# Kernel tuning notes

Hardware: AMD Instinct MI355X
Metric: run time of the kernel (lower is better)

The kernel has to match this reference:

```python
import jax, jax.numpy as jnp
import numpy as np

B, S, HID, H, DK = 16, 1024, 512, 8, 64
NEG = -1e30


def setup_inputs() -> dict:
    key = jax.random.key(0)
    kx, kl, kq, kk, kv, ko = jax.random.split(key, 6)
    x = jax.random.normal(kx, (B, S, HID), dtype=jnp.float32)
    # mask is a prefix of ones per sample (the torch code fills nmask[i, :nsum, :nsum])
    lengths = jax.random.randint(kl, (B,), S // 2, S + 1)
    mask = (jnp.arange(S)[None, :] < lengths[:, None]).astype(jnp.int32)
    scale = 0.02
    Wq = jax.random.normal(kq, (H, HID, DK), dtype=jnp.float32) * scale  # stacked per-head Linear weights
    Wk = jax.random.normal(kk, (H, HID, DK), dtype=jnp.float32) * scale
    Wv = jax.random.normal(kv, (H, HID, DK), dtype=jnp.float32) * scale
    Wout = jax.random.normal(ko, (H * DK, HID), dtype=jnp.float32) * scale
    return {"x": x, "mask": mask, "Wq": Wq, "Wk": Wk, "Wv": Wv, "Wout": Wout}


def reference(x, mask, Wq, Wk, Wv, Wout):
    # x: [B,S,HID], mask: [B,S] int prefix mask
    nsum = mask.sum(-1).astype(jnp.float32)          # [B]
    valid = mask.astype(bool)                         # [B,S]
    pair = valid[:, :, None] & valid[:, None, :]      # [B,S,S] == nmask from the torch loop
    # batched per-head projections (equivalent to the per-head Linear loop)
    Q = jnp.einsum('bsh,nhd->bnsd', x, Wq)            # [B,H,S,DK]
    K = jnp.einsum('bsh,nhd->bnsd', x, Wk)
    V = jnp.einsum('bsh,nhd->bnsd', x, Wv)
    scores = jnp.einsum('bnqd,bnkd->bnqk', Q, K)      # [B,H,S,S]
    scores = scores / jnp.sqrt(nsum)[:, None, None, None]  # per-sample sqrt(len) scale
    scores = jnp.where(pair[:, None, :, :], scores, NEG)   # masked_softmax: -1e30 at masked slots
    p = jax.nn.softmax(scores, axis=-1)
    attn = jnp.einsum('bnqk,bnkd->bnqd', p, V)        # [B,H,S,DK]
    h = attn.transpose(0, 2, 1, 3).reshape(B, S, H * DK)  # concat heads along feature dim
    return jnp.einsum('bsf,fh->bsh', h, Wout)         # W_out, no bias
```

## Files before the change

kernel.cpp:

```cpp
#include <hip/hip_runtime.h>
#include <math.h>

constexpr int CB = 16;
constexpr int CS = 1024;
constexpr int CHID = 512;
constexpr int CH = 8;
constexpr int CDK = 64;

typedef _Float16 f16;
typedef __attribute__((ext_vector_type(8))) _Float16 f16x8;
typedef __attribute__((ext_vector_type(4))) _Float16 f16x4;
typedef __attribute__((ext_vector_type(4))) float f32x4;
typedef __attribute__((ext_vector_type(4))) unsigned int u32x4;
typedef __attribute__((ext_vector_type(2))) unsigned int u32x2;

__device__ inline f32x4 mfma16(f16x8 a, f16x8 b, f32x4 c) {
  return __builtin_amdgcn_mfma_f32_16x16x32_f16(a, b, c, 0, 0, 0);
}

__device__ inline void gld16(const void* g, void* l) {
  __builtin_amdgcn_global_load_lds(
      (const __attribute__((address_space(1))) void*)g,
      (__attribute__((address_space(3))) void*)l, 16, 0, 0);
}

__device__ inline float fast_exp2(float x) {
#if __has_builtin(__builtin_amdgcn_exp2f)
  return __builtin_amdgcn_exp2f(x);
#else
  return __expf(x * 0.6931471805599453f);
#endif
}

__device__ inline unsigned pack_rne(float a, float b) {
  union { f16 h[2]; unsigned u; } c;
  c.h[0] = (f16)a;
  c.h[1] = (f16)b;
  return c.u;
}

__device__ inline void quad_transpose(unsigned& x, unsigned& y) {
#if __has_builtin(__builtin_amdgcn_permlane32_swap) && \
    __has_builtin(__builtin_amdgcn_permlane16_swap)
  u32x2 a = __builtin_amdgcn_permlane32_swap(x, y, false, false);
  u32x2 b = __builtin_amdgcn_permlane16_swap(a[0], a[1], false, false);
  x = b[0];
  y = b[1];
#else
  asm volatile(
      "s_nop 1\n\t"
      "v_permlane32_swap_b32 %0, %1\n\t"
      "s_nop 1\n\t"
      "v_permlane16_swap_b32 %0, %1\n\t"
      "s_nop 1"
      : "+v"(x), "+v"(y));
#endif
}

#define LOG2E 1.4426950408889634f

__global__ __launch_bounds__(256) void prep_kernel(const float4* __restrict__ x,
                                                   f16x4* __restrict__ xh,
                                                   const int* __restrict__ mask,
                                                   int* __restrict__ lens,
                                                   float* __restrict__ Vsum) {
  const int bid = blockIdx.x, t = threadIdx.x;
  __shared__ int red[256];
  if (bid < 8192) {
    const int idx = bid * 256 + t;
    const float4 v = x[idx];
    f16x4 o;
    o[0] = (f16)v.x; o[1] = (f16)v.y; o[2] = (f16)v.z; o[3] = (f16)v.w;
    xh[idx] = o;
  } else {
    const int b = bid - 8192;
    const int g = b * 256 + t;
    Vsum[g * 2] = 0.f;
    Vsum[g * 2 + 1] = 0.f;
    int s = 0;
    for (int i = t; i < CS; i += 256) s += mask[b * CS + i];
    red[t] = s;
    __syncthreads();
    for (int off = 128; off > 0; off >>= 1) {
      if (t < off) red[t] += red[t + off];
      __syncthreads();
    }
    if (t == 0) lens[b] = red[0];
  }
}

__global__ __launch_bounds__(256) void cast_w_kernel(const float* __restrict__ Wq,
                                                     const float* __restrict__ Wk,
                                                     const float* __restrict__ Wv,
                                                     const float* __restrict__ Wout,
                                                     f16* __restrict__ wtAll) {
  const int y = blockIdx.y, kb = blockIdx.x, t = threadIdx.x;
  const int k0 = kb * 64;
  const float* src;
  int ldsrc;
  f16* dst;
  if (y < 24) {
    const int which = y >> 3, h = y & 7;
    const float* W = (which == 0) ? Wq : (which == 1) ? Wk : Wv;
    src = W + (size_t)h * 32768 + (size_t)k0 * 64;
    ldsrc = 64;
    dst = wtAll + (size_t)which * 262144 + (size_t)h * 32768;
  } else {
    const int c = y - 24;
    src = Wout + (size_t)k0 * 512 + c * 64;
    ldsrc = 512;
    dst = wtAll + (size_t)3 * 262144 + (size_t)c * 64 * 512;
  }

  __shared__ float Ts[64][68];
  {
    const int kr = t >> 4, cg = (t & 15) * 4;
#pragma unroll
    for (int rr = 0; rr < 4; ++rr) {
      const float4 v = *(const float4*)&src[(size_t)(rr * 16 + kr) * ldsrc + cg];
      Ts[rr * 16 + kr][cg] = v.x;
      Ts[rr * 16 + kr][cg + 1] = v.y;
      Ts[rr * 16 + kr][cg + 2] = v.z;
      Ts[rr * 16 + kr][cg + 3] = v.w;
    }
  }
  __syncthreads();
  {
    const int n = t >> 2, seg = t & 3;
    f16x8 a, b;
#pragma unroll
    for (int j = 0; j < 8; ++j) {
      a[j] = (f16)Ts[seg * 16 + j][n];
      b[j] = (f16)Ts[seg * 16 + 8 + j][n];
    }
    f16* d = &dst[(size_t)n * 512 + k0 + seg * 16];
    *(f16x8*)d = a;
    *(f16x8*)(d + 8) = b;
  }
}

__global__ __launch_bounds__(256) void qkvf_kernel(
    const f16* __restrict__ xh, const f16* __restrict__ wtAll,
    const int* __restrict__ lens, f16* __restrict__ Qh, f16* __restrict__ Kh,
    f16* __restrict__ Vth, float* __restrict__ Vsum) {
  const int ct = blockIdx.x, rt = blockIdx.y;
  const int which = ct >> 2, hp = ct & 3;
  const f16* Wt = wtAll + (size_t)which * 262144 + (size_t)hp * 65536;
  const int row0 = rt * 128;
  const int b = row0 >> 10, s0 = row0 & 1023;
  const int h0 = hp * 2;
  const int t = threadIdx.x;
  const int w = t >> 6, lane = t & 63, quad = lane >> 4, lcol = lane & 15;
  const int wr = w >> 1, wc = w & 1;

  __shared__ union SM {
    struct { f16 Xs[128][64]; f16 Ws[128][64]; } a;
    f16 Ts[128][136];
  } sm;

  f32x4 acc[4][4];
#pragma unroll
  for (int i = 0; i < 4; ++i)
#pragma unroll
    for (int j = 0; j < 4; ++j) acc[i][j] = (f32x4){0.f, 0.f, 0.f, 0.f};

  for (int k0 = 0; k0 < CHID; k0 += 64) {
    __syncthreads();
#pragma unroll
    for (int i = 0; i < 4; ++i) {
      const int c = t + 256 * i, r = c >> 3, sg = c & 7;
      const int gsw = (sg ^ (r & 7)) * 8;
      gld16(&xh[(size_t)(row0 + r) * CHID + k0 + gsw],
            (char*)&sm.a.Xs[0][0] + c * 16);
      gld16(&Wt[(size_t)r * CHID + k0 + gsw], (char*)&sm.a.Ws[0][0] + c * 16);
    }
    __syncthreads();

    f16x8 bf0[4], bf1[4];
#pragma unroll
    for (int j = 0; j < 4; ++j) {
      const int br = wc * 64 + j * 16 + lcol;
      bf0[j] = *(const f16x8*)&sm.a.Ws[br][(quad ^ (br & 7)) * 8];
      bf1[j] = *(const f16x8*)&sm.a.Ws[br][((quad ^ 4) ^ (br & 7)) * 8];
    }
#pragma unroll
    for (int i = 0; i < 4; ++i) {
      const int ar = wr * 64 + i * 16 + lcol;
      const f16x8 af0 = *(const f16x8*)&sm.a.Xs[ar][(quad ^ (ar & 7)) * 8];
      const f16x8 af1 =
          *(const f16x8*)&sm.a.Xs[ar][((quad ^ 4) ^ (ar & 7)) * 8];
#pragma unroll
      for (int j = 0; j < 4; ++j) {
        acc[i][j] = mfma16(af0, bf0[j], acc[i][j]);
        acc[i][j] = mfma16(af1, bf1[j], acc[i][j]);
      }
    }
  }

  if (which == 2) {
#pragma unroll
    for (int j = 0; j < 4; ++j) {
      float ps = 0.f;
#pragma unroll
      for (int i = 0; i < 4; ++i)
#pragma unroll
        for (int rr = 0; rr < 4; ++rr) ps += acc[i][j][rr];
      ps += __shfl_xor(ps, 16);
      ps += __shfl_xor(ps, 32);
      if (quad == 0) {
        const int d128 = wc * 64 + j * 16 + lcol;
        const int h = h0 + (d128 >> 6), d = d128 & 63;
        atomicAdd(&Vsum[((size_t)b * CH + h) * CDK + d], ps);
      }
    }
    __syncthreads();
#pragma unroll
    for (int i = 0; i < 4; ++i)
#pragma unroll
      for (int j = 0; j < 4; ++j) {
        f16x4 v4;
#pragma unroll
        for (int rr = 0; rr < 4; ++rr) v4[rr] = (f16)acc[i][j][rr];
        *(f16x4*)&sm.Ts[wc * 64 + j * 16 + lcol][wr * 64 + i * 16 + quad * 4] =
            v4;
      }
    __syncthreads();
    const int c16 = t & 15;
#pragma unroll
    for (int p = 0; p < 8; ++p) {
      const int vr = p * 16 + (t >> 4);
      const int h = h0 + (vr >> 6), d = vr & 63;
      *(f16x8*)&Vth[(((size_t)b * CH + h) * CDK + d) * CS + s0 + c16 * 8] =
          *(const f16x8*)&sm.Ts[vr][c16 * 8];
    }
  } else {
    const float qsc = (which == 0) ? rsqrtf((float)lens[b]) * LOG2E : 1.0f;
    __syncthreads();
#pragma unroll
    for (int i = 0; i < 4; ++i)
#pragma unroll
      for (int j = 0; j < 4; ++j)
#pragma unroll
        for (int rr = 0; rr < 4; ++rr)
          sm.Ts[wr * 64 + i * 16 + quad * 4 + rr][wc * 64 + j * 16 + lcol] =
              (f16)(acc[i][j][rr] * qsc);
    __syncthreads();
    f16* O = (which == 0) ? Qh : Kh;
    const int c8 = t & 7;
#pragma unroll
    for (int p = 0; p < 4; ++p) {
      const int row = p * 32 + (t >> 3);
#pragma unroll
      for (int half = 0; half < 2; ++half) {
        const int h = h0 + half;
        *(f16x8*)&O[(((size_t)b * CH + h) * CS + s0 + row) * CDK + c8 * 8] =
            *(const f16x8*)&sm.Ts[row][half * 64 + c8 * 8];
      }
    }
  }
}

__global__ __launch_bounds__(512, 4) void attn_kernel(
    const f16* __restrict__ Qh, const f16* __restrict__ Kh,
    const f16* __restrict__ Vth, const int* __restrict__ lens,
    const float* __restrict__ Vsum, f16* __restrict__ Hbh) {
  const int id = blockIdx.x;
  const int h = id & 7;
  const int slot = id >> 3;
  const int qt = slot & 3;
  const int b = slot >> 2;
  const int n = lens[b];
  const int t = threadIdx.x, w = t >> 6, lane = t & 63, quad = lane >> 4,
            lcol = lane & 15;

  const size_t bh = ((size_t)b * CH + h) * CS;
  const size_t bhd = ((size_t)b * CH + h) * CDK;

  const int nt = (n + 63) >> 6;
  const int rem = n & 63;
  const int ntm = rem ? nt - 1 : nt;

  __shared__ union SM {
    struct { f16 Ks[2][64][72]; f16 Vs[2][64][72]; } kv;
    f16 St[8][32][72];
  } sm;

  const int qbase = qt * 256 + w * 32;
  f16x8 qa[2][2];
#pragma unroll
  for (int set = 0; set < 2; ++set) {
    const size_t qr = bh + qbase + set * 16 + lcol;
    qa[set][0] = *(const f16x8*)&Qh[qr * CDK + quad * 8];
    qa[set][1] = *(const f16x8*)&Qh[qr * CDK + 32 + quad * 8];
  }

  f16x8 vones;
#pragma unroll
  for (int j = 0; j < 8; ++j) vones[j] = (f16)1.0f;

  f32x4 o[2][4];
#pragma unroll
  for (int set = 0; set < 2; ++set)
#pragma unroll
    for (int dt = 0; dt < 4; ++dt) o[set][dt] = (f32x4){0.f, 0.f, 0.f, 0.f};
  f32x4 o_l[2] = {(f32x4){0.f, 0.f, 0.f, 0.f}, (f32x4){0.f, 0.f, 0.f, 0.f}};

  const int sr = t >> 3, sg = t & 7;

  f16x8 pk, pv;
  pk = *(const f16x8*)&Kh[(bh + sr) * CDK + sg * 8];
  pv = *(const f16x8*)&Vth[(bhd + sr) * CS + sg * 8];
  *(f16x8*)&sm.kv.Ks[0][sr][sg * 8] = pk;
  *(f16x8*)&sm.kv.Vs[0][sr][sg * 8] = pv;
  __syncthreads();

  auto ktile = [&](const int kt, const bool masked) __attribute__((always_inline)) {
    const int cur = kt & 1, nxt = cur ^ 1;
    const int ktn = (kt + 1 < nt) ? kt + 1 : kt;
    pk = *(const f16x8*)&Kh[(bh + ktn * 64 + sr) * CDK + sg * 8];
    pv = *(const f16x8*)&Vth[(bhd + sr) * CS + ktn * 64 + sg * 8];

    f16x8 pa[2][2];
#pragma unroll
    for (int set = 0; set < 2; ++set) {
      f32x4 st[4];
#pragma unroll
      for (int ct = 0; ct < 4; ++ct) {
        const f16x8 kb0 = *(const f16x8*)&sm.kv.Ks[cur][ct * 16 + lcol][quad * 8];
        const f16x8 kb1 =
            *(const f16x8*)&sm.kv.Ks[cur][ct * 16 + lcol][32 + quad * 8];
        st[ct] = mfma16(kb0, qa[set][0], (f32x4){0.f, 0.f, 0.f, 0.f});
        st[ct] = mfma16(kb1, qa[set][1], st[ct]);
      }
      unsigned pkd[4][2];
#pragma unroll
      for (int c = 0; c < 4; ++c) {
        float p[4];
#pragma unroll
        for (int r = 0; r < 4; ++r) {
          float e = fast_exp2(st[c][r]);
          if (masked) {
            const bool kvld = (kt * 64 + c * 16 + quad * 4 + r) < n;
            e = kvld ? e : 0.f;
          }
          p[r] = e;
        }
        pkd[c][0] = pack_rne(p[0], p[1]);
        pkd[c][1] = pack_rne(p[2], p[3]);
      }
#pragma unroll
      for (int half = 0; half < 2; ++half) {
        unsigned x0 = pkd[2 * half][0], y0 = pkd[2 * half + 1][0];
        unsigned x1 = pkd[2 * half][1], y1 = pkd[2 * half + 1][1];
        quad_transpose(x0, y0);
        quad_transpose(x1, y1);
        union { u32x4 u; f16x8 h; } cc;
        cc.u = (u32x4){x0, x1, y0, y1};
        pa[set][half] = cc.h;
      }
    }

#pragma unroll
    for (int dt = 0; dt < 4; ++dt) {
      const f16x8 vb0 = *(const f16x8*)&sm.kv.Vs[cur][dt * 16 + lcol][quad * 8];
      const f16x8 vb1 =
          *(const f16x8*)&sm.kv.Vs[cur][dt * 16 + lcol][32 + quad * 8];
#pragma unroll
      for (int set = 0; set < 2; ++set) {
        o[set][dt] = mfma16(pa[set][0], vb0, o[set][dt]);
        o[set][dt] = mfma16(pa[set][1], vb1, o[set][dt]);
      }
    }
#pragma unroll
    for (int set = 0; set < 2; ++set) {
      o_l[set] = mfma16(pa[set][0], vones, o_l[set]);
      o_l[set] = mfma16(pa[set][1], vones, o_l[set]);
    }

    *(f16x8*)&sm.kv.Ks[nxt][sr][sg * 8] = pk;
    *(f16x8*)&sm.kv.Vs[nxt][sr][sg * 8] = pv;
    __syncthreads();
  };

  int kt = 0;
  for (; kt < ntm; ++kt) ktile(kt, false);
  if (rem) ktile(kt, true);

  float invl[2][4];
#pragma unroll
  for (int set = 0; set < 2; ++set)
#pragma unroll
    for (int r = 0; r < 4; ++r) invl[set][r] = 1.0f / o_l[set][r];

#pragma unroll
  for (int set = 0; set < 2; ++set)
#pragma unroll
    for (int dt = 0; dt < 4; ++dt)
#pragma unroll
      for (int r = 0; r < 4; ++r) {
        const int srow_l = set * 16 + quad * 4 + r;
        const int d = dt * 16 + lcol;
        const float val = (qbase + srow_l < n)
                              ? o[set][dt][r] * invl[set][r]
                              : Vsum[bhd + d] * (1.0f / 1024.0f);
        sm.St[w][srow_l][d] = (f16)val;
      }
  {
    const int lr = lane >> 3, lc = lane & 7;
#pragma unroll
    for (int p = 0; p < 4; ++p) {
      const int row = p * 8 + lr;
      *(f16x8*)&Hbh[((size_t)b * CS + qbase + row) * (CH * CDK) + h * CDK +
                    lc * 8] = *(const f16x8*)&sm.St[w][row][lc * 8];
    }
  }
}

__global__ __launch_bounds__(256) void outp_kernel(const f16* __restrict__ Hbh,
                                                   const f16* __restrict__ woutt,
                                                   float* __restrict__ out) {
  const int rt = blockIdx.x, ctile = blockIdx.y;
  const int row0 = rt * 128, col0 = ctile * 128;
  const f16* Wt = woutt + (size_t)col0 * CHID;
  const int t = threadIdx.x;
  const int w = t >> 6, lane = t & 63, quad = lane >> 4, lcol = lane & 15;
  const int wr = w >> 1, wc = w & 1;

  __shared__ f16 Hs[128][64];
  __shared__ f16 Ws[128][64];

  f32x4 acc[4][4];
#pragma unroll
  for (int i = 0; i < 4; ++i)
#pragma unroll
    for (int j = 0; j < 4; ++j) acc[i][j] = (f32x4){0.f, 0.f, 0.f, 0.f};

  for (int k0 = 0; k0 < CHID; k0 += 64) {
    __syncthreads();
#pragma unroll
    for (int i = 0; i < 4; ++i) {
      const int c = t + 256 * i, r = c >> 3, sg = c & 7;
      const int gsw = (sg ^ (r & 7)) * 8;
      gld16(&Hbh[(size_t)(row0 + r) * CHID + k0 + gsw],
            (char*)&Hs[0][0] + c * 16);
      gld16(&Wt[(size_t)r * CHID + k0 + gsw], (char*)&Ws[0][0] + c * 16);
    }
    __syncthreads();

    f16x8 bf0[4], bf1[4];
#pragma unroll
    for (int j = 0; j < 4; ++j) {
      const int br = wc * 64 + j * 16 + lcol;
      bf0[j] = *(const f16x8*)&Ws[br][(quad ^ (br & 7)) * 8];
      bf1[j] = *(const f16x8*)&Ws[br][((quad ^ 4) ^ (br & 7)) * 8];
    }
#pragma unroll
    for (int i = 0; i < 4; ++i) {
      const int ar = wr * 64 + i * 16 + lcol;
      const f16x8 af0 = *(const f16x8*)&Hs[ar][(quad ^ (ar & 7)) * 8];
      const f16x8 af1 = *(const f16x8*)&Hs[ar][((quad ^ 4) ^ (ar & 7)) * 8];
#pragma unroll
      for (int j = 0; j < 4; ++j) {
        acc[i][j] = mfma16(af0, bf0[j], acc[i][j]);
        acc[i][j] = mfma16(af1, bf1[j], acc[i][j]);
      }
    }
  }

#pragma unroll
  for (int i = 0; i < 4; ++i) {
#pragma unroll
    for (int rr = 0; rr < 4; ++rr) {
      const size_t rg = row0 + wr * 64 + i * 16 + quad * 4 + rr;
#pragma unroll
      for (int j = 0; j < 4; ++j)
        out[rg * CHID + col0 + wc * 64 + j * 16 + lcol] = acc[i][j][rr];
    }
  }
}

extern "C" void kernel_launch(void* const* d_in, const int* in_sizes, int n_in,
                              void* d_out, int out_size, void* d_ws,
                              size_t ws_size, hipStream_t stream) {
  const float* x = (const float*)d_in[0];
  const int* mask = (const int*)d_in[1];
  const float* Wq = (const float*)d_in[2];
  const float* Wk = (const float*)d_in[3];
  const float* Wv = (const float*)d_in[4];
  const float* Wout = (const float*)d_in[5];
  float* out = (float*)d_out;

  char* ws = (char*)d_ws;
  int* lens = (int*)ws;
  size_t off = 1024;
  const size_t NX = (size_t)CB * CS * CHID;
  const size_t NW = (size_t)CH * CHID * CDK;
  f16* xh = (f16*)(ws + off);    off += NX * 2;
  f16* wtAll = (f16*)(ws + off); off += NW * 4 * 2;
  f16* Qh = (f16*)(ws + off);    off += NX * 2;
  f16* Kh = (f16*)(ws + off);    off += NX * 2;
  f16* Vth = (f16*)(ws + off);   off += NX * 2;
  f16* Hbh = (f16*)(ws + off);   off += NX * 2;
  float* Vsum = (float*)(ws + off); off += (size_t)CB * CH * CDK * 4;
  f16* woutt = wtAll + NW * 3;

  prep_kernel<<<8208, 256, 0, stream>>>((const float4*)x, (f16x4*)xh, mask,
                                        lens, Vsum);
  cast_w_kernel<<<dim3(8, 32), 256, 0, stream>>>(Wq, Wk, Wv, Wout, wtAll);
  qkvf_kernel<<<dim3(12, 128), 256, 0, stream>>>(xh, wtAll, lens, Qh, Kh, Vth,
                                                 Vsum);
  attn_kernel<<<512, 512, 0, stream>>>(Qh, Kh, Vth, lens, Vsum, Hbh);
  outp_kernel<<<dim3(128, 4), 256, 0, stream>>>(Hbh, woutt, out);
}
```

Measured before the change: 192.4 us.

## Load K/V tiles directly from global into registers, drop LDS staging

The attention kernel no longer stages K and V tiles through double-buffered shared memory with a barrier per tile. Each wave now reads its MFMA operands straight from global memory, relying on L1/L2 to serve the reuse across waves. Blocks shrink from 512 to 256 threads (128 query rows each) and the grid doubles to 1024. This removes LDS traffic and per-tile __syncthreads, but every wave issues redundant global loads for the same K/V tile, and those loads are no longer prefetched a tile ahead.

```diff
diff --git a/kernel.cpp b/kernel.cpp
--- a/kernel.cpp
+++ b/kernel.cpp
@@ -260,15 +260,15 @@
   }
 }
 
-__global__ __launch_bounds__(512, 4) void attn_kernel(
+__global__ __launch_bounds__(256, 3) void attn_kernel(
     const f16* __restrict__ Qh, const f16* __restrict__ Kh,
     const f16* __restrict__ Vth, const int* __restrict__ lens,
     const float* __restrict__ Vsum, f16* __restrict__ Hbh) {
   const int id = blockIdx.x;
   const int h = id & 7;
-  const int slot = id >> 3;
-  const int qt = slot & 3;
-  const int b = slot >> 2;
+  const int rest = id >> 3;
+  const int qt = rest & 7;
+  const int b = rest >> 3;
   const int n = lens[b];
   const int t = threadIdx.x, w = t >> 6, lane = t & 63, quad = lane >> 4,
             lcol = lane & 15;
@@ -280,12 +280,9 @@
   const int rem = n & 63;
   const int ntm = rem ? nt - 1 : nt;
 
-  __shared__ union SM {
-    struct { f16 Ks[2][64][72]; f16 Vs[2][64][72]; } kv;
-    f16 St[8][32][72];
-  } sm;
-
-  const int qbase = qt * 256 + w * 32;
+  __shared__ f16 St[4][32][72];
+
+  const int qbase = qt * 128 + w * 32;
   f16x8 qa[2][2];
 #pragma unroll
   for (int set = 0; set < 2; ++set) {
@@ -305,20 +302,17 @@
     for (int dt = 0; dt < 4; ++dt) o[set][dt] = (f32x4){0.f, 0.f, 0.f, 0.f};
   f32x4 o_l[2] = {(f32x4){0.f, 0.f, 0.f, 0.f}, (f32x4){0.f, 0.f, 0.f, 0.f}};
 
-  const int sr = t >> 3, sg = t & 7;
-
-  f16x8 pk, pv;
-  pk = *(const f16x8*)&Kh[(bh + sr) * CDK + sg * 8];
-  pv = *(const f16x8*)&Vth[(bhd + sr) * CS + sg * 8];
-  *(f16x8*)&sm.kv.Ks[0][sr][sg * 8] = pk;
-  *(f16x8*)&sm.kv.Vs[0][sr][sg * 8] = pv;
-  __syncthreads();
+  const f16* Kp = &Kh[(bh + lcol) * CDK + quad * 8];
+  const f16* Vp = &Vth[(bhd + lcol) * CS + quad * 8];
 
   auto ktile = [&](const int kt, const bool masked) __attribute__((always_inline)) {
-    const int cur = kt & 1, nxt = cur ^ 1;
-    const int ktn = (kt + 1 < nt) ? kt + 1 : kt;
-    pk = *(const f16x8*)&Kh[(bh + ktn * 64 + sr) * CDK + sg * 8];
-    pv = *(const f16x8*)&Vth[(bhd + sr) * CS + ktn * 64 + sg * 8];
+    const f16* Kt = Kp + (size_t)kt * 64 * CDK;
+    f16x8 kb[4][2];
+#pragma unroll
+    for (int ct = 0; ct < 4; ++ct) {
+      kb[ct][0] = *(const f16x8*)(Kt + (size_t)ct * 16 * CDK);
+      kb[ct][1] = *(const f16x8*)(Kt + (size_t)ct * 16 * CDK + 32);
+    }
 
     f16x8 pa[2][2];
 #pragma unroll
@@ -326,11 +320,8 @@
       f32x4 st[4];
 #pragma unroll
       for (int ct = 0; ct < 4; ++ct) {
-        const f16x8 kb0 = *(const f16x8*)&sm.kv.Ks[cur][ct * 16 + lcol][quad * 8];
-        const f16x8 kb1 =
-            *(const f16x8*)&sm.kv.Ks[cur][ct * 16 + lcol][32 + quad * 8];
-        st[ct] = mfma16(kb0, qa[set][0], (f32x4){0.f, 0.f, 0.f, 0.f});
-        st[ct] = mfma16(kb1, qa[set][1], st[ct]);
+        st[ct] = mfma16(kb[ct][0], qa[set][0], (f32x4){0.f, 0.f, 0.f, 0.f});
+        st[ct] = mfma16(kb[ct][1], qa[set][1], st[ct]);
       }
       unsigned pkd[4][2];
 #pragma unroll
@@ -360,11 +351,11 @@
       }
     }
 
+    const f16* Vt = Vp + (size_t)kt * 64;
 #pragma unroll
     for (int dt = 0; dt < 4; ++dt) {
-      const f16x8 vb0 = *(const f16x8*)&sm.kv.Vs[cur][dt * 16 + lcol][quad * 8];
-      const f16x8 vb1 =
-          *(const f16x8*)&sm.kv.Vs[cur][dt * 16 + lcol][32 + quad * 8];
+      const f16x8 vb0 = *(const f16x8*)(Vt + (size_t)dt * 16 * CS);
+      const f16x8 vb1 = *(const f16x8*)(Vt + (size_t)dt * 16 * CS + 32);
 #pragma unroll
       for (int set = 0; set < 2; ++set) {
         o[set][dt] = mfma16(pa[set][0], vb0, o[set][dt]);
@@ -376,10 +367,6 @@
       o_l[set] = mfma16(pa[set][0], vones, o_l[set]);
       o_l[set] = mfma16(pa[set][1], vones, o_l[set]);
     }
-
-    *(f16x8*)&sm.kv.Ks[nxt][sr][sg * 8] = pk;
-    *(f16x8*)&sm.kv.Vs[nxt][sr][sg * 8] = pv;
-    __syncthreads();
   };
 
   int kt = 0;
@@ -403,7 +390,7 @@
         const float val = (qbase + srow_l < n)
                               ? o[set][dt][r] * invl[set][r]
                               : Vsum[bhd + d] * (1.0f / 1024.0f);
-        sm.St[w][srow_l][d] = (f16)val;
+        St[w][srow_l][d] = (f16)val;
       }
   {
     const int lr = lane >> 3, lc = lane & 7;
@@ -411,7 +398,7 @@
     for (int p = 0; p < 4; ++p) {
       const int row = p * 8 + lr;
       *(f16x8*)&Hbh[((size_t)b * CS + qbase + row) * (CH * CDK) + h * CDK +
-                    lc * 8] = *(const f16x8*)&sm.St[w][row][lc * 8];
+                    lc * 8] = *(const f16x8*)&St[w][row][lc * 8];
     }
   }
 }
@@ -509,6 +496,6 @@
   cast_w_kernel<<<dim3(8, 32), 256, 0, stream>>>(Wq, Wk, Wv, Wout, wtAll);
   qkvf_kernel<<<dim3(12, 128), 256, 0, stream>>>(xh, wtAll, lens, Qh, Kh, Vth,
                                                  Vsum);
-  attn_kernel<<<512, 512, 0, stream>>>(Qh, Kh, Vth, lens, Vsum, Hbh);
+  attn_kernel<<<1024, 256, 0, stream>>>(Qh, Kh, Vth, lens, Vsum, Hbh);
   outp_kernel<<<dim3(128, 4), 256, 0, stream>>>(Hbh, woutt, out);
 }
```

Result: slower. 247.7 us (+28.8%).
